# Kernel tuning notes

Measured on AMD Instinct MI355X. Metric: run time of the kernel, lower is better.

Reference implementation:

```python
import jax, jax.numpy as jnp
import numpy as np

# Dimensions (match init_kwargs)
N, B = 32, 16384            # num_elements (agents), batch_size
SD, AD, AD2 = 128, 64, 64   # state_dim, action_dim, action_dim2
IDIM = SD + AD              # per-agent encoder input (obs + act)
H, HEADS = 256, 4           # hidden_dim, attend_heads
AT = H // HEADS             # attend_dim = 64
ODIM = AD                   # critic output = action_dim


def setup_inputs() -> dict:
    key = jax.random.key(0)
    ks = jax.random.split(key, 20)
    g = lambda k, shape: (jax.random.normal(k, shape, jnp.float32) * 0.05)
    return {
        "agent_inputs": jax.random.normal(ks[0], (N, B, IDIM), jnp.float32),
        "state_agent": jax.random.normal(ks[1], (B, SD), jnp.float32),
        "meanfield": jax.random.normal(ks[2], (B, AD), jnp.float32),
        "meanfield2": jax.random.normal(ks[3], (B, AD2), jnp.float32),
        # per-agent critic encoders (enc_fc1)
        "enc_W": g(ks[4], (N, IDIM, H)), "enc_b": g(ks[5], (N, H)),
        # state / meanfield / meanfield2 encoders
        "sW": g(ks[6], (SD, H)), "sb": g(ks[7], (H,)),
        "mfW": g(ks[8], (AD, H)), "mfb": g(ks[9], (H,)),
        "mf2W": g(ks[10], (AD2, H)), "mf2b": g(ks[11], (H,)),
        # per-head key / selector (bias-free) and value extractors
        "Wk": g(ks[12], (HEADS, H, AT)),
        "Wsel": g(ks[13], (HEADS, H, AT)),
        "Wv": g(ks[14], (HEADS, H, AT)), "bv": g(ks[15], (HEADS, AT)),
        # critic head: Linear(4H->H) + LeakyReLU + Linear(H->odim)
        "W1": g(ks[16], (4 * H, H)), "b1": g(ks[17], (H,)),
        "W2": g(ks[18], (H, ODIM)), "b2": g(ks[19], (ODIM,)),
    }


def reference(agent_inputs, state_agent, meanfield, meanfield2,
              enc_W, enc_b, sW, sb, mfW, mfb, mf2W, mf2b,
              Wk, Wsel, Wv, bv, W1, b1, W2, b2):
    lrelu = jax.nn.leaky_relu  # default negative_slope=0.01, matches nn.LeakyReLU
    # Per-agent (obs,act) encoders: [N,B,H]
    sa = lrelu(jnp.einsum('nbi,nih->nbh', agent_inputs, enc_W) + enc_b[:, None, :])
    s_enc = lrelu(state_agent @ sW + sb)          # [B,H]
    mf_enc = lrelu(meanfield @ mfW + mfb)         # [B,H]
    mf2_enc = lrelu(meanfield2 @ mf2W + mf2b)     # [B,H]
    # agents = [0]; keys/values come from all agents except agent 0
    others = sa[1:]                               # [N-1,B,H]
    keys = jnp.einsum('nbh,ehd->enbd', others, Wk)                       # [E,N-1,B,AT]
    vals = lrelu(jnp.einsum('nbh,ehd->enbd', others, Wv) + bv[:, None, None, :])
    sel = jnp.einsum('bh,ehd->ebd', s_enc, Wsel)                         # [E,B,AT]
    logits = jnp.einsum('ebd,enbd->ebn', sel, keys) / jnp.sqrt(jnp.float32(AT))
    w = jax.nn.softmax(logits, axis=-1)                                  # over N-1 agents
    other_vals = jnp.einsum('ebn,enbd->ebd', w, vals)                    # [E,B,AT]
    # concatenate heads in order, matching torch cat over per-head results
    other_flat = jnp.transpose(other_vals, (1, 0, 2)).reshape(B, HEADS * AT)
    critic_in = jnp.concatenate([s_enc, mf_enc, mf2_enc, other_flat], axis=1)  # [B,4H]
    h1 = lrelu(critic_in @ W1 + b1)
    return h1 @ W2 + b2                                                  # all_q: [B,ODIM]
```

## Files before the change

kernel.cpp:

```cpp
#include <hip/hip_runtime.h>
#include <hip/hip_bf16.h>

#define N_AG   32
#define B_SZ   16384
#define SD_    128
#define AD_    64
#define IDIM_  192
#define H_     256
#define HEADS_ 4
#define AT_    64
#define NO_    31

typedef __attribute__((ext_vector_type(8))) short bf16x8_t;
typedef __attribute__((ext_vector_type(4))) float f32x4_t;
typedef __attribute__((ext_vector_type(4))) unsigned int u32x4_t;

__device__ inline unsigned short f2bfu(float f){
  union { __hip_bfloat16 h; unsigned short u; } cv;
  cv.h = __float2bfloat16(f);
  return cv.u;
}
__device__ inline float bflo(unsigned int u){
  union { float f; unsigned int i; } c; c.i = u << 16; return c.f;
}
__device__ inline float bfhi(unsigned int u){
  union { float f; unsigned int i; } c; c.i = u & 0xffff0000u; return c.f;
}

__device__ inline void gll16(const unsigned short* g, unsigned short* l) {
  __builtin_amdgcn_global_load_lds(
      (const __attribute__((address_space(1))) unsigned int*)g,
      (__attribute__((address_space(3))) unsigned int*)l, 16, 0, 0);
}

__device__ inline float dot8(bf16x8_t a, bf16x8_t b, float acc){
  u32x4_t au = __builtin_bit_cast(u32x4_t, a);
  u32x4_t bu = __builtin_bit_cast(u32x4_t, b);
  #pragma unroll
  for (int i = 0; i < 4; i++) {
    acc = fmaf(bflo(au[i]), bflo(bu[i]), acc);
    acc = fmaf(bfhi(au[i]), bfhi(bu[i]), acc);
  }
  return acc;
}

__global__ __launch_bounds__(256) void k_prep(
    const float* __restrict__ encW, const float* __restrict__ sW,
    const float* __restrict__ mfW,  const float* __restrict__ mf2W,
    const float* __restrict__ W1,   const float* __restrict__ W2,
    const float* __restrict__ Wv,   const float* __restrict__ Wsel,
    const float* __restrict__ Wk,
    unsigned short* __restrict__ encWt, unsigned short* __restrict__ sWt,
    unsigned short* __restrict__ mfWt,  unsigned short* __restrict__ mf2Wt,
    unsigned short* __restrict__ W1t,   unsigned short* __restrict__ W2t,
    unsigned short* __restrict__ WvT,   unsigned short* __restrict__ Mct)
{
  const int bid = blockIdx.x, tid = threadIdx.x;
  auto tr = [&](const float* src, unsigned short* dst, int K, int N, int idx){
    int kn = K * N;
    int b = idx / kn, i = idx - b * kn;
    int n = i / K, k = i - n * K;
    dst[(long)b * kn + i] = f2bfu(src[(long)b * kn + (long)k * N + n]);
  };
  if (bid < 5952)        tr(encW + 192*256, encWt, 192, 256, bid*256 + tid);
  else if (bid < 6080)   tr(sW,   sWt,  128, 256, (bid-5952)*256 + tid);
  else if (bid < 6144)   tr(mfW,  mfWt,  64, 256, (bid-6080)*256 + tid);
  else if (bid < 6208)   tr(mf2W, mf2Wt, 64, 256, (bid-6144)*256 + tid);
  else if (bid < 7232)   tr(W1,   W1t, 1024, 256, (bid-6208)*256 + tid);
  else if (bid < 7296)   tr(W2,   W2t,  256,  64, (bid-7232)*256 + tid);
  else if (bid < 7552)   tr(Wv,   WvT,  256,  64, (bid-7296)*256 + tid);
  else {
    int idx = (bid - 7552) * 256 + tid;
    int hp = idx & 255, eh = idx >> 8;
    int e = eh >> 8, h = eh & 255;
    const float* ws = Wsel + ((long)e * 256 + hp) * 64;
    const float* wk = Wk   + ((long)e * 256 + h ) * 64;
    float s = 0.f;
    #pragma unroll 8
    for (int d = 0; d < 64; d++) s += ws[d] * wk[d];
    Mct[idx] = f2bfu(0.125f * s);
  }
}

template<bool AF32, bool LRELU, bool OUTF32>
__global__ __launch_bounds__(512, 2) void k_gemm2(
    const void* __restrict__ Ap, int lda, long strideA,
    const unsigned short* __restrict__ Bt, long strideB,
    const float* __restrict__ bias, long strideBias,
    void* __restrict__ Cp, int ldc, long strideC,
    int K)
{
  __shared__ __align__(16) unsigned short Alds[2][64 * 64];
  __shared__ __align__(16) unsigned short Blds[2][256 * 64];

  const int tid = threadIdx.x;
  const int lane = tid & 63, w = tid >> 6;
  const int wr = w >> 2, wc = w & 3;
  const int lr = lane & 15, lg = lane >> 4;
  const int bm = blockIdx.x, bn = blockIdx.y, bz = blockIdx.z;

  f32x4_t acc[2][4];
  #pragma unroll
  for (int i = 0; i < 2; i++)
    #pragma unroll
    for (int j = 0; j < 4; j++) acc[i][j] = (f32x4_t){0.f, 0.f, 0.f, 0.f};

  const unsigned short* Bb = Bt + bz * strideB + (long)(bn * 256) * K;
  const float* Af32 = AF32 ? (const float*)Ap + bz * strideA + (long)(bm * 64) * lda : nullptr;
  const unsigned short* Abf = AF32 ? nullptr
      : (const unsigned short*)Ap + bz * strideA + (long)(bm * 64) * lda;
  const int nt = K >> 6;

  float4 ar0, ar1;

  auto stageB = [&](int buf, int k0){
    #pragma unroll
    for (int i = 0; i < 4; i++) {
      int c = i * 512 + tid;
      int n = c >> 3, sl = c & 7;
      gll16(Bb + (long)n * K + k0 + (((sl ^ (n & 7)) & 7) << 3), &Blds[buf][c * 8]);
    }
  };
  auto issueA = [&](int buf, int k0){
    if (AF32) {
      int r0 = tid >> 4, q0 = tid & 15;
      ar0 = *reinterpret_cast<const float4*>(Af32 + (long)r0 * lda + k0 + q0 * 4);
      int c1 = tid + 512, r1 = c1 >> 4, q1 = c1 & 15;
      ar1 = *reinterpret_cast<const float4*>(Af32 + (long)r1 * lda + k0 + q1 * 4);
    } else {
      int row = tid >> 3, sl = tid & 7;
      gll16(Abf + (long)row * lda + k0 + (((sl ^ (row & 7)) & 7) << 3),
            &Alds[buf][tid * 8]);
    }
  };
  auto writeA = [&](int buf){
    if (AF32) {
      {
        int c = tid, row = c >> 4, q = c & 15;
        ushort4 u;
        u.x = f2bfu(ar0.x); u.y = f2bfu(ar0.y); u.z = f2bfu(ar0.z); u.w = f2bfu(ar0.w);
        int di = row * 64 + ((((q >> 1) ^ (row & 7)) & 7) << 3) + ((q & 1) << 2);
        *reinterpret_cast<ushort4*>(&Alds[buf][di]) = u;
      }
      {
        int c = tid + 512, row = c >> 4, q = c & 15;
        ushort4 u;
        u.x = f2bfu(ar1.x); u.y = f2bfu(ar1.y); u.z = f2bfu(ar1.z); u.w = f2bfu(ar1.w);
        int di = row * 64 + ((((q >> 1) ^ (row & 7)) & 7) << 3) + ((q & 1) << 2);
        *reinterpret_cast<ushort4*>(&Alds[buf][di]) = u;
      }
    }
  };

  issueA(0, 0);
  stageB(0, 0);
  writeA(0);

  for (int t = 0; t < nt; t++) {
    const int cur = t & 1;
    asm volatile("s_waitcnt vmcnt(0) lgkmcnt(0)" ::: "memory");
    __builtin_amdgcn_s_barrier();
    __builtin_amdgcn_sched_barrier(0);
    if (t + 1 < nt) { issueA(cur ^ 1, (t + 1) * 64); stageB(cur ^ 1, (t + 1) * 64); }
    __builtin_amdgcn_sched_barrier(0);

    bf16x8_t af[2][2], bf[4][2];
    #pragma unroll
    for (int mf = 0; mf < 2; mf++)
      #pragma unroll
      for (int kk = 0; kk < 2; kk++) {
        int row = wr * 32 + mf * 16 + lr;
        af[mf][kk] = *reinterpret_cast<const bf16x8_t*>(
            &Alds[cur][row * 64 + ((((kk * 4 + lg) ^ (row & 7)) & 7) << 3)]);
      }
    #pragma unroll
    for (int nf = 0; nf < 4; nf++)
      #pragma unroll
      for (int kk = 0; kk < 2; kk++) {
        int n = wc * 64 + nf * 16 + lr;
        bf[nf][kk] = *reinterpret_cast<const bf16x8_t*>(
            &Blds[cur][n * 64 + ((((kk * 4 + lg) ^ (n & 7)) & 7) << 3)]);
      }
    #pragma unroll
    for (int kk = 0; kk < 2; kk++)
      #pragma unroll
      for (int mf = 0; mf < 2; mf++)
        #pragma unroll
        for (int nf = 0; nf < 4; nf++)
          acc[mf][nf] = __builtin_amdgcn_mfma_f32_16x16x32_bf16(af[mf][kk], bf[nf][kk], acc[mf][nf], 0, 0, 0);

    __builtin_amdgcn_sched_barrier(0);
    if (t + 1 < nt) writeA(cur ^ 1);
  }

  const float* bp = bias ? bias + bz * strideBias : nullptr;
  #pragma unroll
  for (int nf = 0; nf < 4; nf++) {
    int col = bn * 256 + wc * 64 + nf * 16 + lr;
    float bvv = bp ? bp[col] : 0.f;
    #pragma unroll
    for (int mf = 0; mf < 2; mf++) {
      #pragma unroll
      for (int r = 0; r < 4; r++) {
        int row = bm * 64 + wr * 32 + mf * 16 + lg * 4 + r;
        float v = acc[mf][nf][r] + bvv;
        if (LRELU) v = v > 0.f ? v : 0.01f * v;
        if (OUTF32)
          ((float*)Cp)[bz * strideC + (long)row * ldc + col] = v;
        else
          ((unsigned short*)Cp)[bz * strideC + (long)row * ldc + col] = f2bfu(v);
      }
    }
  }
}

__global__ __launch_bounds__(512) void k_attnw(
    const unsigned short* __restrict__ others,
    const unsigned short* __restrict__ qbuf,
    float* __restrict__ wbuf,
    float* __restrict__ wsum)
{
  __shared__ __align__(16) unsigned short olds[2][16 * 256];

  const int tid = threadIdx.x;
  const int bm = blockIdx.x;
  const int row = tid >> 5, sub = tid & 31;
  const int e = sub >> 3, ch = sub & 7;
  const long grow = (long)bm * 16 + row;

  bf16x8_t qr[4];
  #pragma unroll
  for (int j = 0; j < 4; j++)
    qr[j] = *reinterpret_cast<const bf16x8_t*>(
        &qbuf[grow * 1024 + e * 256 + ch * 32 + j * 8]);

  float psum = 0.f;

  auto stage = [&](int buf, int n){
    int r = tid >> 5, slot = tid & 31;
    gll16(others + ((long)(bm * 16 + r) * NO_ + n) * 256 + ((slot ^ ((r & 7) << 2)) << 3),
          &olds[buf][tid * 8]);
  };

  stage(0, 0);

  for (int n = 0; n < NO_; n++) {
    const int cur = n & 1;
    __syncthreads();
    if (n + 1 < NO_) stage(cur ^ 1, n + 1);

    float d = 0.f;
    #pragma unroll
    for (int j = 0; j < 4; j++) {
      int slot = (ch * 4 + j) ^ ((row & 7) << 2);
      bf16x8_t o8 = *reinterpret_cast<const bf16x8_t*>(&olds[cur][row * 256 + slot * 8]);
      d = dot8(o8, qr[j], d);
    }
    d += __shfl_xor(d, 1);
    d += __shfl_xor(d, 2);
    d += __shfl_xor(d, 4);
    float p = __expf(d);
    psum += p;
    if (ch == 0) wbuf[grow * 124 + e * 31 + n] = p;
  }
  if (ch == 0) wsum[grow * 4 + e] = psum;
}

__global__ __launch_bounds__(512) void k_pv(
    const unsigned short* __restrict__ others,
    const unsigned short* __restrict__ WvT,
    const float* __restrict__ wbuf,
    const float* __restrict__ wsum,
    const float* __restrict__ bv,
    unsigned short* __restrict__ critic)
{
  __shared__ __align__(16) unsigned short olds[2][16 * 256];
  __shared__ float pl[2][64];

  const int tid = threadIdx.x;
  const int lane = tid & 63, w = tid >> 6;
  const int lr = lane & 15, lg = lane >> 4;
  const int bm = blockIdx.x;
  const int e = w >> 1;

  bf16x8_t wv[2][8];
  #pragma unroll
  for (int nf = 0; nf < 2; nf++)
    #pragma unroll
    for (int kk = 0; kk < 8; kk++)
      wv[nf][kk] = *reinterpret_cast<const bf16x8_t*>(
          &WvT[(long)(w * 32 + nf * 16 + lr) * 256 + kk * 32 + lg * 8]);
  float bvv[2] = { bv[w * 32 + lr], bv[w * 32 + 16 + lr] };

  f32x4_t outa[2];
  outa[0] = (f32x4_t){0.f, 0.f, 0.f, 0.f};
  outa[1] = (f32x4_t){0.f, 0.f, 0.f, 0.f};

  auto stage = [&](int buf, int n){
    int r = tid >> 5, slot = tid & 31;
    gll16(others + ((long)(bm * 16 + r) * NO_ + n) * 256 + ((slot ^ ((r & 7) << 2)) << 3),
          &olds[buf][tid * 8]);
  };
  auto stagep = [&](int buf, int n){
    if (tid < 64)
      pl[buf][tid] = wbuf[((long)bm * 16 + (tid >> 2)) * 124 + (tid & 3) * 31 + n];
  };

  stage(0, 0); stagep(0, 0);

  for (int n = 0; n < NO_; n++) {
    const int cur = n & 1;
    __syncthreads();
    if (n + 1 < NO_) { stage(cur ^ 1, n + 1); stagep(cur ^ 1, n + 1); }

    f32x4_t va[2];
    va[0] = (f32x4_t){0.f, 0.f, 0.f, 0.f};
    va[1] = (f32x4_t){0.f, 0.f, 0.f, 0.f};
    #pragma unroll
    for (int kk = 0; kk < 8; kk++) {
      bf16x8_t af = *reinterpret_cast<const bf16x8_t*>(
          &olds[cur][lr * 256 + (((kk * 4 + lg) ^ ((lr & 7) << 2)) << 3)]);
      va[0] = __builtin_amdgcn_mfma_f32_16x16x32_bf16(af, wv[0][kk], va[0], 0, 0, 0);
      va[1] = __builtin_amdgcn_mfma_f32_16x16x32_bf16(af, wv[1][kk], va[1], 0, 0, 0);
    }

    #pragma unroll
    for (int r = 0; r < 4; r++) {
      float p = pl[cur][(lg * 4 + r) * 4 + e];
      #pragma unroll
      for (int nf = 0; nf < 2; nf++) {
        float v = va[nf][r] + bvv[nf];
        v = v > 0.f ? v : 0.01f * v;
        outa[nf][r] += p * v;
      }
    }
  }

  #pragma unroll
  for (int r = 0; r < 4; r++) {
    long grow = (long)bm * 16 + lg * 4 + r;
    float inv = 1.f / wsum[grow * 4 + e];
    #pragma unroll
    for (int nf = 0; nf < 2; nf++)
      critic[grow * 1024 + 768 + w * 32 + nf * 16 + lr] = f2bfu(outa[nf][r] * inv);
  }
}

template<bool AF32, bool LRELU, bool OUTF32>
__global__ __launch_bounds__(256) void k_gemm(
    const void* __restrict__ Ap, int lda, long strideA,
    const unsigned short* __restrict__ Bt, long strideB,
    const float* __restrict__ bias, long strideBias,
    void* __restrict__ Cp, int ldc, long strideC,
    int K)
{
  __shared__ __align__(16) unsigned short Alds[128][40];
  __shared__ __align__(16) unsigned short Blds[64][40];

  const int tid = threadIdx.x;
  const int bm = blockIdx.x, bn = blockIdx.y, bz = blockIdx.z;
  const int w = tid >> 6, lane = tid & 63;
  const int wr = (w >> 1) * 64, wc = (w & 1) * 32;
  const int lr = lane & 15, lk = (lane >> 4) * 8;

  f32x4_t acc[4][2];
  #pragma unroll
  for (int i = 0; i < 4; i++)
    #pragma unroll
    for (int j = 0; j < 2; j++) acc[i][j] = (f32x4_t){0.f, 0.f, 0.f, 0.f};

  const unsigned short* Bb = Bt + bz * strideB + (long)(bn * 64) * K;

  for (int k0 = 0; k0 < K; k0 += 32) {
    if (AF32) {
      const float* A = (const float*)Ap + bz * strideA + (long)(bm * 128) * lda + k0;
      #pragma unroll
      for (int i = 0; i < 4; i++) {
        int chunk = tid + i * 256;
        int m = chunk >> 3, kc = (chunk & 7) * 4;
        const float4 v = *reinterpret_cast<const float4*>(A + (long)m * lda + kc);
        ushort4 p;
        p.x = f2bfu(v.x); p.y = f2bfu(v.y); p.z = f2bfu(v.z); p.w = f2bfu(v.w);
        *reinterpret_cast<ushort4*>(&Alds[m][kc]) = p;
      }
    } else {
      const unsigned short* A = (const unsigned short*)Ap + bz * strideA + (long)(bm * 128) * lda + k0;
      #pragma unroll
      for (int i = 0; i < 4; i++) {
        int chunk = tid + i * 256;
        int m = chunk >> 3, kc = (chunk & 7) * 4;
        *reinterpret_cast<ushort4*>(&Alds[m][kc]) =
            *reinterpret_cast<const ushort4*>(A + (long)m * lda + kc);
      }
    }
    #pragma unroll
    for (int i = 0; i < 2; i++) {
      int chunk = tid + i * 256;
      int n = chunk >> 3, kc = (chunk & 7) * 4;
      *reinterpret_cast<ushort4*>(&Blds[n][kc]) =
          *reinterpret_cast<const ushort4*>(Bb + (long)n * K + k0 + kc);
    }
    __syncthreads();

    bf16x8_t bfr0 = *reinterpret_cast<const bf16x8_t*>(&Blds[wc + lr][lk]);
    bf16x8_t bfr1 = *reinterpret_cast<const bf16x8_t*>(&Blds[wc + 16 + lr][lk]);
    #pragma unroll
    for (int mf = 0; mf < 4; mf++) {
      bf16x8_t afr = *reinterpret_cast<const bf16x8_t*>(&Alds[wr + mf * 16 + lr][lk]);
      acc[mf][0] = __builtin_amdgcn_mfma_f32_16x16x32_bf16(afr, bfr0, acc[mf][0], 0, 0, 0);
      acc[mf][1] = __builtin_amdgcn_mfma_f32_16x16x32_bf16(afr, bfr1, acc[mf][1], 0, 0, 0);
    }
    __syncthreads();
  }

  const float* bp = bias ? bias + bz * strideBias : nullptr;
  #pragma unroll
  for (int nf = 0; nf < 2; nf++) {
    int col = bn * 64 + wc + nf * 16 + lr;
    float bvv = bp ? bp[col] : 0.f;
    #pragma unroll
    for (int mf = 0; mf < 4; mf++) {
      #pragma unroll
      for (int r = 0; r < 4; r++) {
        int row = bm * 128 + wr + mf * 16 + (lane >> 4) * 4 + r;
        float v = acc[mf][nf][r] + bvv;
        if (LRELU) v = v > 0.f ? v : 0.01f * v;
        if (OUTF32)
          ((float*)Cp)[bz * strideC + (long)row * ldc + col] = v;
        else
          ((unsigned short*)Cp)[bz * strideC + (long)row * ldc + col] = f2bfu(v);
      }
    }
  }
}

extern "C" void kernel_launch(void* const* d_in, const int* in_sizes, int n_in,
                              void* d_out, int out_size, void* d_ws, size_t ws_size,
                              hipStream_t stream)
{
  (void)in_sizes; (void)n_in; (void)out_size; (void)ws_size;
  const float* agent = (const float*)d_in[0];
  const float* state = (const float*)d_in[1];
  const float* mf    = (const float*)d_in[2];
  const float* mf2   = (const float*)d_in[3];
  const float* encW  = (const float*)d_in[4];
  const float* encb  = (const float*)d_in[5];
  const float* sW    = (const float*)d_in[6];
  const float* sb    = (const float*)d_in[7];
  const float* mfW   = (const float*)d_in[8];
  const float* mfb   = (const float*)d_in[9];
  const float* mf2W  = (const float*)d_in[10];
  const float* mf2b  = (const float*)d_in[11];
  const float* Wk    = (const float*)d_in[12];
  const float* Wsel  = (const float*)d_in[13];
  const float* Wv    = (const float*)d_in[14];
  const float* bv    = (const float*)d_in[15];
  const float* W1    = (const float*)d_in[16];
  const float* b1    = (const float*)d_in[17];
  const float* W2    = (const float*)d_in[18];
  const float* b2    = (const float*)d_in[19];
  float* out = (float*)d_out;

  char* ws = (char*)d_ws;
  size_t off = 0;
  auto alloc = [&](size_t bytes) -> char* {
    char* p = ws + off; off += (bytes + 255) & ~(size_t)255; return p;
  };
  unsigned short* others = (unsigned short*)alloc((size_t)B_SZ * NO_ * H_ * 2);
  unsigned short* qbuf   = (unsigned short*)alloc((size_t)B_SZ * 1024 * 2);
  unsigned short* critic = (unsigned short*)alloc((size_t)B_SZ * 1024 * 2);
  unsigned short* h1buf  = (unsigned short*)alloc((size_t)B_SZ * H_ * 2);
  float*          wbuf   = (float*)alloc((size_t)B_SZ * HEADS_ * NO_ * 4);
  float*          wsum   = (float*)alloc((size_t)B_SZ * HEADS_ * 4);
  unsigned short* encWt  = (unsigned short*)alloc((size_t)NO_ * H_ * IDIM_ * 2);
  unsigned short* Mct    = (unsigned short*)alloc((size_t)1024 * 256 * 2);
  unsigned short* WvT    = (unsigned short*)alloc((size_t)256 * 256 * 2);
  unsigned short* sWt    = (unsigned short*)alloc((size_t)256 * 128 * 2);
  unsigned short* mfWt   = (unsigned short*)alloc((size_t)256 * 64 * 2);
  unsigned short* mf2Wt  = (unsigned short*)alloc((size_t)256 * 64 * 2);
  unsigned short* W1t    = (unsigned short*)alloc((size_t)256 * 1024 * 2);
  unsigned short* W2t    = (unsigned short*)alloc((size_t)64 * 256 * 2);

  k_prep<<<dim3(8576), 256, 0, stream>>>(
      encW, sW, mfW, mf2W, W1, W2, Wv, Wsel, Wk,
      encWt, sWt, mfWt, mf2Wt, W1t, W2t, WvT, Mct);

  k_gemm2<true, true, false><<<dim3(256, 1, NO_), 512, 0, stream>>>(
      agent + (size_t)B_SZ * IDIM_, IDIM_, (long)B_SZ * IDIM_,
      encWt, (long)H_ * IDIM_,
      encb + H_, H_,
      others, NO_ * H_, H_, IDIM_);

  k_gemm2<true, true, false><<<dim3(256, 1, 1), 512, 0, stream>>>(
      state, SD_, 0, sWt, 0, sb, 0, critic, 1024, 0, SD_);
  k_gemm2<true, true, false><<<dim3(256, 1, 1), 512, 0, stream>>>(
      mf, AD_, 0, mfWt, 0, mfb, 0, critic + 256, 1024, 0, AD_);
  k_gemm2<true, true, false><<<dim3(256, 1, 1), 512, 0, stream>>>(
      mf2, AD_, 0, mf2Wt, 0, mf2b, 0, critic + 512, 1024, 0, AD_);

  k_gemm2<false, false, false><<<dim3(256, 4, 1), 512, 0, stream>>>(
      critic, 1024, 0, Mct, 0, nullptr, 0, qbuf, 1024, 0, 256);

  k_attnw<<<dim3(B_SZ / 16), 512, 0, stream>>>(others, qbuf, wbuf, wsum);

  k_pv<<<dim3(B_SZ / 16), 512, 0, stream>>>(others, WvT, wbuf, wsum, bv, critic);

  k_gemm2<false, true, false><<<dim3(256, 1, 1), 512, 0, stream>>>(
      critic, 1024, 0, W1t, 0, b1, 0, h1buf, H_, 0, 1024);

  k_gemm<false, false, true><<<dim3(128, 1, 1), 256, 0, stream>>>(
      h1buf, H_, 0, W2t, 0, b2, 0, out, 64, 0, 256);
}
```

Before: 448.5 us.

## Process 32 batch rows per block in attention-weight and PV kernels

Both attention kernels now handle 32 batch rows per 512-thread block instead of 16, so the grid is half as large. k_pv reuses its register-resident Wv fragments across two 16-row MFMA tiles, and k_attnw gives each thread a longer dot product with one fewer shuffle step. The aim is to amortize per-block setup (Wv fragment loads, q loads) and barriers over more work. In exchange, shared memory per block doubles to 32 KB, register pressure rises, and only 512 blocks remain to spread across the CUs.

```diff
diff --git a/kernel.cpp b/kernel.cpp
--- a/kernel.cpp
+++ b/kernel.cpp
@@ -220,26 +220,30 @@
     float* __restrict__ wbuf,
     float* __restrict__ wsum)
 {
-  __shared__ __align__(16) unsigned short olds[2][16 * 256];
+  __shared__ __align__(16) unsigned short olds[2][32 * 256];
 
   const int tid = threadIdx.x;
   const int bm = blockIdx.x;
-  const int row = tid >> 5, sub = tid & 31;
-  const int e = sub >> 3, ch = sub & 7;
-  const long grow = (long)bm * 16 + row;
-
-  bf16x8_t qr[4];
-  #pragma unroll
-  for (int j = 0; j < 4; j++)
+  const int row = tid >> 4, sub = tid & 15;
+  const int e = sub >> 2, ch = sub & 3;
+  const long grow = (long)bm * 32 + row;
+
+  bf16x8_t qr[8];
+  #pragma unroll
+  for (int j = 0; j < 8; j++)
     qr[j] = *reinterpret_cast<const bf16x8_t*>(
-        &qbuf[grow * 1024 + e * 256 + ch * 32 + j * 8]);
+        &qbuf[grow * 1024 + e * 256 + ch * 64 + j * 8]);
 
   float psum = 0.f;
 
   auto stage = [&](int buf, int n){
-    int r = tid >> 5, slot = tid & 31;
-    gll16(others + ((long)(bm * 16 + r) * NO_ + n) * 256 + ((slot ^ ((r & 7) << 2)) << 3),
-          &olds[buf][tid * 8]);
+    #pragma unroll
+    for (int i = 0; i < 2; i++) {
+      int c = i * 512 + tid;
+      int r = c >> 5, slot = c & 31;
+      gll16(others + ((long)(bm * 32 + r) * NO_ + n) * 256 + ((slot ^ ((r & 7) << 2)) << 3),
+            &olds[buf][c * 8]);
+    }
   };
 
   stage(0, 0);
@@ -251,14 +255,13 @@
 
     float d = 0.f;
     #pragma unroll
-    for (int j = 0; j < 4; j++) {
-      int slot = (ch * 4 + j) ^ ((row & 7) << 2);
+    for (int j = 0; j < 8; j++) {
+      int slot = (ch * 8 + j) ^ ((row & 7) << 2);
       bf16x8_t o8 = *reinterpret_cast<const bf16x8_t*>(&olds[cur][row * 256 + slot * 8]);
       d = dot8(o8, qr[j], d);
     }
     d += __shfl_xor(d, 1);
     d += __shfl_xor(d, 2);
-    d += __shfl_xor(d, 4);
     float p = __expf(d);
     psum += p;
     if (ch == 0) wbuf[grow * 124 + e * 31 + n] = p;
@@ -274,8 +277,8 @@
     const float* __restrict__ bv,
     unsigned short* __restrict__ critic)
 {
-  __shared__ __align__(16) unsigned short olds[2][16 * 256];
-  __shared__ float pl[2][64];
+  __shared__ __align__(16) unsigned short olds[2][32 * 256];
+  __shared__ float pl[2][128];
 
   const int tid = threadIdx.x;
   const int lane = tid & 63, w = tid >> 6;
@@ -292,18 +295,24 @@
           &WvT[(long)(w * 32 + nf * 16 + lr) * 256 + kk * 32 + lg * 8]);
   float bvv[2] = { bv[w * 32 + lr], bv[w * 32 + 16 + lr] };
 
-  f32x4_t outa[2];
-  outa[0] = (f32x4_t){0.f, 0.f, 0.f, 0.f};
-  outa[1] = (f32x4_t){0.f, 0.f, 0.f, 0.f};
+  f32x4_t outa[2][2];
+  #pragma unroll
+  for (int mf = 0; mf < 2; mf++)
+    #pragma unroll
+    for (int nf = 0; nf < 2; nf++) outa[mf][nf] = (f32x4_t){0.f, 0.f, 0.f, 0.f};
 
   auto stage = [&](int buf, int n){
-    int r = tid >> 5, slot = tid & 31;
-    gll16(others + ((long)(bm * 16 + r) * NO_ + n) * 256 + ((slot ^ ((r & 7) << 2)) << 3),
-          &olds[buf][tid * 8]);
+    #pragma unroll
+    for (int i = 0; i < 2; i++) {
+      int c = i * 512 + tid;
+      int r = c >> 5, slot = c & 31;
+      gll16(others + ((long)(bm * 32 + r) * NO_ + n) * 256 + ((slot ^ ((r & 7) << 2)) << 3),
+            &olds[buf][c * 8]);
+    }
   };
   auto stagep = [&](int buf, int n){
-    if (tid < 64)
-      pl[buf][tid] = wbuf[((long)bm * 16 + (tid >> 2)) * 124 + (tid & 3) * 31 + n];
+    if (tid < 128)
+      pl[buf][tid] = wbuf[((long)bm * 32 + (tid >> 2)) * 124 + (tid & 3) * 31 + n];
   };
 
   stage(0, 0); stagep(0, 0);
@@ -313,36 +322,48 @@
     __syncthreads();
     if (n + 1 < NO_) { stage(cur ^ 1, n + 1); stagep(cur ^ 1, n + 1); }
 
-    f32x4_t va[2];
-    va[0] = (f32x4_t){0.f, 0.f, 0.f, 0.f};
-    va[1] = (f32x4_t){0.f, 0.f, 0.f, 0.f};
+    f32x4_t va[2][2];
+    #pragma unroll
+    for (int mf = 0; mf < 2; mf++)
+      #pragma unroll
+      for (int nf = 0; nf < 2; nf++) va[mf][nf] = (f32x4_t){0.f, 0.f, 0.f, 0.f};
     #pragma unroll
     for (int kk = 0; kk < 8; kk++) {
-      bf16x8_t af = *reinterpret_cast<const bf16x8_t*>(
+      bf16x8_t af0 = *reinterpret_cast<const bf16x8_t*>(
           &olds[cur][lr * 256 + (((kk * 4 + lg) ^ ((lr & 7) << 2)) << 3)]);
-      va[0] = __builtin_amdgcn_mfma_f32_16x16x32_bf16(af, wv[0][kk], va[0], 0, 0, 0);
-      va[1] = __builtin_amdgcn_mfma_f32_16x16x32_bf16(af, wv[1][kk], va[1], 0, 0, 0);
-    }
-
+      bf16x8_t af1 = *reinterpret_cast<const bf16x8_t*>(
+          &olds[cur][(16 + lr) * 256 + (((kk * 4 + lg) ^ ((lr & 7) << 2)) << 3)]);
+      va[0][0] = __builtin_amdgcn_mfma_f32_16x16x32_bf16(af0, wv[0][kk], va[0][0], 0, 0, 0);
+      va[0][1] = __builtin_amdgcn_mfma_f32_16x16x32_bf16(af0, wv[1][kk], va[0][1], 0, 0, 0);
+      va[1][0] = __builtin_amdgcn_mfma_f32_16x16x32_bf16(af1, wv[0][kk], va[1][0], 0, 0, 0);
+      va[1][1] = __builtin_amdgcn_mfma_f32_16x16x32_bf16(af1, wv[1][kk], va[1][1], 0, 0, 0);
+    }
+
+    #pragma unroll
+    for (int mf = 0; mf < 2; mf++) {
+      #pragma unroll
+      for (int r = 0; r < 4; r++) {
+        float p = pl[cur][(mf * 16 + lg * 4 + r) * 4 + e];
+        #pragma unroll
+        for (int nf = 0; nf < 2; nf++) {
+          float v = va[mf][nf][r] + bvv[nf];
+          v = v > 0.f ? v : 0.01f * v;
+          outa[mf][nf][r] += p * v;
+        }
+      }
+    }
+  }
+
+  #pragma unroll
+  for (int mf = 0; mf < 2; mf++) {
     #pragma unroll
     for (int r = 0; r < 4; r++) {
-      float p = pl[cur][(lg * 4 + r) * 4 + e];
-      #pragma unroll
-      for (int nf = 0; nf < 2; nf++) {
-        float v = va[nf][r] + bvv[nf];
-        v = v > 0.f ? v : 0.01f * v;
-        outa[nf][r] += p * v;
-      }
-    }
-  }
-
-  #pragma unroll
-  for (int r = 0; r < 4; r++) {
-    long grow = (long)bm * 16 + lg * 4 + r;
-    float inv = 1.f / wsum[grow * 4 + e];
-    #pragma unroll
-    for (int nf = 0; nf < 2; nf++)
-      critic[grow * 1024 + 768 + w * 32 + nf * 16 + lr] = f2bfu(outa[nf][r] * inv);
+      long grow = (long)bm * 32 + mf * 16 + lg * 4 + r;
+      float inv = 1.f / wsum[grow * 4 + e];
+      #pragma unroll
+      for (int nf = 0; nf < 2; nf++)
+        critic[grow * 1024 + 768 + w * 32 + nf * 16 + lr] = f2bfu(outa[mf][nf][r] * inv);
+    }
   }
 }
 
@@ -501,9 +522,9 @@
   k_gemm2<false, false, false><<<dim3(256, 4, 1), 512, 0, stream>>>(
       critic, 1024, 0, Mct, 0, nullptr, 0, qbuf, 1024, 0, 256);
 
-  k_attnw<<<dim3(B_SZ / 16), 512, 0, stream>>>(others, qbuf, wbuf, wsum);
-
-  k_pv<<<dim3(B_SZ / 16), 512, 0, stream>>>(others, WvT, wbuf, wsum, bv, critic);
+  k_attnw<<<dim3(B_SZ / 32), 512, 0, stream>>>(others, qbuf, wbuf, wsum);
+
+  k_pv<<<dim3(B_SZ / 32), 512, 0, stream>>>(others, WvT, wbuf, wsum, bv, critic);
 
   k_gemm2<false, true, false><<<dim3(256, 1, 1), 512, 0, stream>>>(
       critic, 1024, 0, W1t, 0, b1, 0, h1buf, H_, 0, 1024);
```

Result: slower. 466.6 us (+4.0%).
